# Kernel tuning notes

Hardware: AMD Instinct MI355X
Metric: run time of the kernel (lower is better)

## Reference

```python
import jax, jax.numpy as jnp
import numpy as np

# S6Layer dims: d_model=256; internal d_state=max(8,16//2)=8; expand=max(1.5,2*0.75)=1.5 -> d_inner=384
B, L, DM = 8, 4096, 256
DI, DS = 384, 8
CHUNK = 32  # seq_len > 64 path: chunked scan, state resets to 0 at every chunk (faithful to source)
EPS = 1e-5


def setup_inputs() -> dict:
    key = jax.random.key(0)
    ks = jax.random.split(key, 8)
    def w(k, shape, s=0.02):
        return jax.random.normal(k, shape, jnp.float32) * s
    return {
        "x": jax.random.normal(ks[0], (B, L, DM), jnp.float32),
        "gamma": jnp.ones((DM,), jnp.float32),
        "beta": jnp.zeros((DM,), jnp.float32),
        "W_in": w(ks[1], (3 * DI, DM)),
        "b_in": jnp.zeros((3 * DI,), jnp.float32),
        "W_dt": w(ks[2], (DI, DI)),
        "b_dt": jnp.zeros((DI,), jnp.float32),
        "A_log": jax.random.normal(ks[3], (DI, DS), jnp.float32),
        "D_vec": jax.random.normal(ks[4], (DI,), jnp.float32),
        "W_out": w(ks[5], (DM, DI)),
        "b_out": jnp.zeros((DM,), jnp.float32),
    }


def _layernorm(x, g, b):
    mu = jnp.mean(x, axis=-1, keepdims=True)
    var = jnp.mean(jnp.square(x - mu), axis=-1, keepdims=True)
    return (x - mu) * jax.lax.rsqrt(var + EPS) * g + b


def _chunked_scan(xp, dt, A):
    # xp, dt: [B, L, DI]; A: [DI, DS]. Each CHUNK-length block scans from h=0
    # (the torch code never propagates h across chunks for seq_len > 64).
    C = L // CHUNK
    xr = xp.reshape(B, C, CHUNK, DI)
    dtr = dt.reshape(B, C, CHUNK, DI)
    dA = jnp.exp(dtr[..., None] * A)              # [B, C, T, DI, DS]
    dA_t = jnp.moveaxis(dA, 2, 0)                 # [T, B, C, DI, DS]
    x_t = jnp.moveaxis(xr, 2, 0)                  # [T, B, C, DI]

    def step(h, inp):
        dA_i, x_i = inp
        h = h * dA_i + x_i[..., None]             # broadcast x over DS
        return h, jnp.sum(h, axis=-1)             # y_i: [B, C, DI]

    h0 = jnp.zeros((B, C, DI, DS), xp.dtype)
    _, ys = jax.lax.scan(step, h0, (dA_t, x_t))   # ys: [T, B, C, DI]
    return jnp.moveaxis(ys, 0, 2).reshape(B, L, DI)


def reference(x, gamma, beta, W_in, b_in, W_dt, b_dt, A_log, D_vec, W_out, b_out):
    residual = x
    xn = _layernorm(x, gamma, beta)
    xz = xn @ W_in.T + b_in                       # [B, L, 3*DI]
    x_proj, z, dt_in = jnp.split(xz, 3, axis=-1)
    x_proj = jax.nn.silu(x_proj)
    z = jax.nn.silu(z)
    dt = jax.nn.softplus(dt_in @ W_dt.T + b_dt)   # [B, L, DI]
    A = -jnp.exp(A_log)                           # [DI, DS]
    y = _chunked_scan(x_proj, dt, A)
    y = y * z + x_proj * D_vec
    return y @ W_out.T + b_out + residual
```

## Files before the change

### kernel.cpp

```cpp
#include <hip/hip_runtime.h>
#include <stdint.h>

#define B_  8
#define L_  4096
#define DM  256
#define DI  384
#define DS  8
#define M_  (B_*L_)

typedef float f32x4 __attribute__((ext_vector_type(4)));
typedef short s16x8 __attribute__((ext_vector_type(8)));

#define AS1(p) ((__attribute__((address_space(1))) void*)(p))
#define AS3(p) ((__attribute__((address_space(3))) void*)(p))

__device__ __forceinline__ unsigned short f2bf(float f) {
  union { float f; uint32_t u; } v; v.f = f;
  uint32_t r = v.u + 0x7FFFu + ((v.u >> 16) & 1u);
  return (unsigned short)(r >> 16);
}
__device__ __forceinline__ float bf2f(unsigned short h) {
  union { uint32_t u; float f; } v; v.u = ((uint32_t)h) << 16;
  return v.f;
}
__device__ __forceinline__ float silu_f(float x) {
  return x * __builtin_amdgcn_rcpf(1.f + __expf(-x));
}

__global__ __launch_bounds__(256) void cvt_kernel(
    const float* __restrict__ w0, const float* __restrict__ w2,
    const float* __restrict__ b_in,
    unsigned short* __restrict__ o0, unsigned short* __restrict__ o2,
    float* __restrict__ biasc) {
  int i = blockIdx.x * 256 + threadIdx.x;
  if (i < 3*DI*DM) o0[i] = f2bf(w0[i]);
  if (i < DM*DI)   o2[i] = f2bf(w2[i]);
  if (i < 2*DI)    biasc[i] = b_in[i];
}

__global__ __launch_bounds__(256) void prep_kernel(
    const float* __restrict__ W_in, const float* __restrict__ b_in,
    const float* __restrict__ W_dt, const float* __restrict__ b_dt,
    unsigned short* __restrict__ winb, float* __restrict__ biasc) {
  int nb = blockIdx.x;
  if (nb < DI) {
    int c = threadIdx.x;
    float acc = 0.f;
    for (int k = 0; k < DI; ++k)
      acc += W_dt[(size_t)nb*DI + k] * W_in[(size_t)(2*DI + k)*DM + c];
    winb[(size_t)(2*DI + nb)*DM + c] = f2bf(acc);
  } else {
    int n = (nb - DI)*256 + threadIdx.x;
    if (n < DI) {
      float acc = b_dt[n];
      for (int k = 0; k < DI; ++k)
        acc += W_dt[(size_t)n*DI + k] * b_in[2*DI + k];
      biasc[2*DI + n] = acc;
    }
  }
}

__global__ __launch_bounds__(256) void ln_kernel(
    const float* __restrict__ x, const float* __restrict__ gamma, const float* __restrict__ beta,
    unsigned short* __restrict__ xn) {
  int token = blockIdx.x * 4 + (threadIdx.x >> 6);
  int lane  = threadIdx.x & 63;
  const float4 v = *(const float4*)(x + (size_t)token*DM + lane*4);
  float s  = v.x + v.y + v.z + v.w;
  float ss = v.x*v.x + v.y*v.y + v.z*v.z + v.w*v.w;
  #pragma unroll
  for (int off = 32; off > 0; off >>= 1) {
    s  += __shfl_xor(s,  off, 64);
    ss += __shfl_xor(ss, off, 64);
  }
  float mean = s * (1.f/DM);
  float var  = ss * (1.f/DM) - mean*mean;
  float rstd = rsqrtf(var + 1e-5f);
  const float4 g = *(const float4*)(gamma + lane*4);
  const float4 b = *(const float4*)(beta  + lane*4);
  ushort4 o;
  o.x = f2bf((v.x - mean)*rstd*g.x + b.x);
  o.y = f2bf((v.y - mean)*rstd*g.y + b.y);
  o.z = f2bf((v.z - mean)*rstd*g.z + b.z);
  o.w = f2bf((v.w - mean)*rstd*g.w + b.w);
  *(ushort4*)(xn + (size_t)token*DM + lane*4) = o;
}

__global__ __launch_bounds__(256, 2) void s6_head(
    const unsigned short* __restrict__ xn,
    const unsigned short* __restrict__ Wb,
    const float* __restrict__ biasc,
    const float* __restrict__ A_log, const float* __restrict__ D_vec,
    unsigned short* __restrict__ yz)
{
  constexpr int K = 256, CPR = K/8;
  __shared__ unsigned short sB[64*K];
  __shared__ unsigned short sOut[3][128*64];
  const int t    = threadIdx.x;
  const int lane = t & 63;
  const int w    = t >> 6;
  const int fr   = lane & 15;
  const int fq   = lane >> 4;
  const int wm   = w * 32;

  const int q      = blockIdx.x;
  const int u      = q >> 3;
  const int mtile  = (q & 7) * 32 + (u & 31);
  const int panel  = u >> 5;
  const int mbase  = mtile * 128;
  const int chbase = panel * 64;

  const unsigned short* gA0 = xn + (size_t)(mbase + wm + fr)*K + fq*8;
  const unsigned short* gA1 = gA0 + (size_t)16*K;
  const unsigned short* sBrE = sB + (size_t)fr*K + ( fq      ^ (fr & 7))*8;
  const unsigned short* sBrO = sB + (size_t)fr*K + ((fq | 4) ^ (fr & 7))*8;

  auto STAGE = [&](int sub) {
    const int nb = sub*DI + chbase;
    #pragma unroll
    for (int i = 0; i < (64*CPR)/256; ++i) {
      int c   = i*256 + t;
      int row = c / CPR;
      int j   = c - row*CPR;
      int jp  = (j & ~7) | ((j & 7) ^ (row & 7));
      __builtin_amdgcn_global_load_lds(AS1(Wb + (size_t)(nb + row)*K + jp*8),
                                       AS3(sB + c*8), 16, 0, 0);
    }
  };
  auto KLOOP = [&](f32x4 (&acc)[2][4]) {
    #pragma unroll
    for (int mi = 0; mi < 2; ++mi)
      #pragma unroll
      for (int ni = 0; ni < 4; ++ni) acc[mi][ni] = (f32x4){0.f, 0.f, 0.f, 0.f};
    #pragma unroll
    for (int kt = 0; kt < 8; ++kt) {
      s16x8 a0 = *(const s16x8*)(gA0 + kt*32);
      s16x8 a1 = *(const s16x8*)(gA1 + kt*32);
      const unsigned short* bb = (kt & 1) ? sBrO : sBrE;
      s16x8 bfr[4];
      #pragma unroll
      for (int ni = 0; ni < 4; ++ni)
        bfr[ni] = *(const s16x8*)(bb + ni*16*K + (kt >> 1)*64);
      #pragma unroll
      for (int ni = 0; ni < 4; ++ni) {
        acc[0][ni] = __builtin_amdgcn_mfma_f32_16x16x32_bf16(a0, bfr[ni], acc[0][ni], 0, 0, 0);
        acc[1][ni] = __builtin_amdgcn_mfma_f32_16x16x32_bf16(a1, bfr[ni], acc[1][ni], 0, 0, 0);
      }
    }
  };
  auto EPI = [&](f32x4 (&acc)[2][4], int sub) {
    const int nb = sub*DI + chbase;
    const bool sl = (sub < 2);
    #pragma unroll
    for (int ni = 0; ni < 4; ++ni) {
      float bv = biasc[nb + ni*16 + fr];
      int cn = (ni*16 + fr) ^ (fq << 4);
      #pragma unroll
      for (int mi = 0; mi < 2; ++mi) {
        int rm0 = wm + mi*16 + fq*4;
        #pragma unroll
        for (int r = 0; r < 4; ++r) {
          float c = acc[mi][ni][r] + bv;
          c = sl ? silu_f(c) : ((c > 20.f) ? c : __logf(1.f + __expf(c)));
          sOut[sub][(rm0 + r)*64 + cn] = f2bf(c);
        }
      }
    }
  };

  f32x4 aP[2][4], aC[2][4];
  STAGE(0);
  __syncthreads();
  KLOOP(aP);
  __syncthreads();
  STAGE(1);
  EPI(aP, 0);
  __syncthreads();
  KLOOP(aC);
  __syncthreads();
  STAGE(2);
  EPI(aC, 1);
  __syncthreads();
  KLOOP(aP);
  EPI(aP, 2);
  __syncthreads();

  {
    const int c  = t >> 6;
    const int d  = t & 63;
    const int ch = chbase + d;
    float a[DS], h[DS];
    #pragma unroll
    for (int s = 0; s < DS; ++s) { a[s] = -__expf(A_log[ch*DS + s]); h[s] = 0.f; }
    float Dv = D_vec[ch];
    unsigned short* yzp = yz + (size_t)(mbase + c*32)*DI + ch;
    for (int tt = 0; tt < 32; ++tt) {
      int idx = (c*32 + tt)*64 + (d ^ (((tt >> 2) & 3) << 4));
      float xv  = bf2f(sOut[0][idx]);
      float zv  = bf2f(sOut[1][idx]);
      float dtv = bf2f(sOut[2][idx]);
      float y = 0.f;
      #pragma unroll
      for (int s = 0; s < DS; ++s) {
        h[s] = h[s] * __expf(dtv * a[s]) + xv;
        y += h[s];
      }
      yzp[(size_t)tt*DI] = f2bf(y * zv + xv * Dv);
    }
  }
}

__global__ __launch_bounds__(256, 3) void gemm_out(
    const unsigned short* __restrict__ A,
    const unsigned short* __restrict__ Bw,
    const float* __restrict__ bias,
    const float* __restrict__ resid, float* __restrict__ o_f)
{
  constexpr int K = 384, CPR = K/8;
  __shared__ unsigned short sB[64*K];
  float* sC = (float*)sB;

  const int t    = threadIdx.x;
  const int lane = t & 63;
  const int w    = t >> 6;
  const int fr   = lane & 15;
  const int fq   = lane >> 4;
  const int wm   = w * 32;

  const int q    = blockIdx.y * 256 + blockIdx.x;
  const int bx2  = (q & 7) * 32 + ((q >> 3) & 31);
  const int by2  = q >> 8;
  const int mbase = bx2 * 128;
  const int nbase = by2 * 64;

  #pragma unroll
  for (int i = 0; i < (64*CPR)/256; ++i) {
    int c   = i*256 + t;
    int row = c / CPR;
    int j   = c - row*CPR;
    int jp  = (j & ~7) | ((j & 7) ^ (row & 7));
    __builtin_amdgcn_global_load_lds(AS1(Bw + (size_t)(nbase + row)*K + jp*8),
                                     AS3(sB + c*8), 16, 0, 0);
  }

  const unsigned short* sBrE = sB + (size_t)fr*K + ( fq      ^ (fr & 7))*8;
  const unsigned short* sBrO = sB + (size_t)fr*K + ((fq | 4) ^ (fr & 7))*8;

  float bvv[4];
  #pragma unroll
  for (int ni = 0; ni < 4; ++ni) bvv[ni] = bias[nbase + ni*16 + fr];

  __syncthreads();

  const unsigned short* gA0 = A + (size_t)(mbase + wm + fr)*K + fq*8;
  const unsigned short* gA1 = gA0 + (size_t)16*K;

  f32x4 acc[2][4];
  #pragma unroll
  for (int mi = 0; mi < 2; ++mi)
    #pragma unroll
    for (int ni = 0; ni < 4; ++ni) acc[mi][ni] = (f32x4){0.f, 0.f, 0.f, 0.f};

  #pragma unroll
  for (int kt = 0; kt < 12; ++kt) {
    s16x8 a0 = *(const s16x8*)(gA0 + kt*32);
    s16x8 a1 = *(const s16x8*)(gA1 + kt*32);
    const unsigned short* bb = (kt & 1) ? sBrO : sBrE;
    s16x8 bfr[4];
    #pragma unroll
    for (int ni = 0; ni < 4; ++ni)
      bfr[ni] = *(const s16x8*)(bb + ni*16*K + (kt >> 1)*64);
    #pragma unroll
    for (int ni = 0; ni < 4; ++ni) {
      acc[0][ni] = __builtin_amdgcn_mfma_f32_16x16x32_bf16(a0, bfr[ni], acc[0][ni], 0, 0, 0);
      acc[1][ni] = __builtin_amdgcn_mfma_f32_16x16x32_bf16(a1, bfr[ni], acc[1][ni], 0, 0, 0);
    }
  }

  __syncthreads();

  #pragma unroll
  for (int ni = 0; ni < 4; ++ni)
    #pragma unroll
    for (int mi = 0; mi < 2; ++mi)
      #pragma unroll
      for (int r = 0; r < 4; ++r)
        sC[(wm + mi*16 + fq*4 + r)*72 + ni*16 + fr] = acc[mi][ni][r] + bvv[ni];

  __syncthreads();

  const int rr = t >> 4, cl = (t & 15) * 4;
  #pragma unroll
  for (int it = 0; it < 8; ++it) {
    int row = rr + it*16;
    const float4 c  = *(const float4*)&sC[row*72 + cl];
    const float4 rv = *(const float4*)(resid + (size_t)(mbase + row)*DM + nbase + cl);
    float4 o;
    o.x = c.x + rv.x; o.y = c.y + rv.y; o.z = c.z + rv.z; o.w = c.w + rv.w;
    *(float4*)(o_f + (size_t)(mbase + row)*DM + nbase + cl) = o;
  }
}

extern "C" void kernel_launch(void* const* d_in, const int* in_sizes, int n_in,
                              void* d_out, int out_size, void* d_ws, size_t ws_size,
                              hipStream_t stream) {
  const float* x     = (const float*)d_in[0];
  const float* gamma = (const float*)d_in[1];
  const float* beta  = (const float*)d_in[2];
  const float* W_in  = (const float*)d_in[3];
  const float* b_in  = (const float*)d_in[4];
  const float* W_dt  = (const float*)d_in[5];
  const float* b_dt  = (const float*)d_in[6];
  const float* A_log = (const float*)d_in[7];
  const float* D_vec = (const float*)d_in[8];
  const float* W_out = (const float*)d_in[9];
  const float* b_out = (const float*)d_in[10];
  float* out = (float*)d_out;

  char* ws = (char*)d_ws;
  size_t off = 0;
  auto alloc = [&](size_t bytes) -> char* {
    char* p = ws + off; off += (bytes + 255) & ~(size_t)255; return p;
  };
  unsigned short* xn    = (unsigned short*)alloc((size_t)M_*DM*2);
  unsigned short* yzb   = (unsigned short*)alloc((size_t)M_*DI*2);
  unsigned short* winb  = (unsigned short*)alloc((size_t)3*DI*DM*2);
  unsigned short* woutb = (unsigned short*)alloc((size_t)DM*DI*2);
  float*          biasc = (float*)alloc((size_t)3*DI*4);

  cvt_kernel<<<dim3((3*DI*DM + 255)/256), 256, 0, stream>>>(W_in, W_out, b_in, winb, woutb, biasc);
  prep_kernel<<<dim3(DI + 2), 256, 0, stream>>>(W_in, b_in, W_dt, b_dt, winb, biasc);
  ln_kernel<<<dim3(M_/4), 256, 0, stream>>>(x, gamma, beta, xn);
  s6_head<<<dim3(6 * 256), 256, 0, stream>>>(xn, winb, biasc, A_log, D_vec, yzb);
  gemm_out<<<dim3(256, DM/64), 256, 0, stream>>>(yzb, woutb, b_out, x, out);
}
```

Baseline: 209.8 us.

## Split-K weight fusion prep, preload A fragments, use exp2 in scan

The serial prep kernel that folds W_dt into W_in (384-step dot per thread) is split into a 4-way split-K kernel plus a reduction kernel, so the preprocessing runs on more blocks with shorter dependency chains. In s6_head, the A-operand fragments are loaded once into registers and reused across the three GEMM sub-passes instead of being reloaded from global memory each time. The scan uses exp2f with A prescaled by log2(e). These changes add an extra launch, scratch memory, and more register pressure in s6_head.

```diff
diff --git a/kernel.cpp b/kernel.cpp
--- a/kernel.cpp
+++ b/kernel.cpp
@@ -38,26 +38,43 @@
   if (i < 2*DI)    biasc[i] = b_in[i];
 }
 
-__global__ __launch_bounds__(256) void prep_kernel(
+__global__ __launch_bounds__(256) void prep1_kernel(
     const float* __restrict__ W_in, const float* __restrict__ b_in,
-    const float* __restrict__ W_dt, const float* __restrict__ b_dt,
+    const float* __restrict__ W_dt,
+    float* __restrict__ scr, float* __restrict__ bscr) {
+  const int n  = blockIdx.x;
+  const int kc = blockIdx.y;
+  const int c  = threadIdx.x;
+  const int kb = kc * 96;
+  const float* wd = W_dt + (size_t)n*DI + kb;
+  const float* wi = W_in + (size_t)(2*DI + kb)*DM + c;
+  float p0 = 0.f, p1 = 0.f, p2 = 0.f, p3 = 0.f;
+  #pragma unroll
+  for (int k = 0; k < 96; k += 4) {
+    p0 += wd[k+0] * wi[(size_t)(k+0)*DM];
+    p1 += wd[k+1] * wi[(size_t)(k+1)*DM];
+    p2 += wd[k+2] * wi[(size_t)(k+2)*DM];
+    p3 += wd[k+3] * wi[(size_t)(k+3)*DM];
+  }
+  scr[(size_t)(n*4 + kc)*256 + c] = (p0 + p1) + (p2 + p3);
+  if (c < 64) {
+    float p = wd[c] * b_in[2*DI + kb + c];
+    if (c < 32) p += wd[64 + c] * b_in[2*DI + kb + 64 + c];
+    #pragma unroll
+    for (int off = 32; off > 0; off >>= 1) p += __shfl_down(p, off, 64);
+    if (c == 0) bscr[n*4 + kc] = p;
+  }
+}
+
+__global__ __launch_bounds__(256) void prep2_kernel(
+    const float* __restrict__ scr, const float* __restrict__ bscr,
+    const float* __restrict__ b_dt,
     unsigned short* __restrict__ winb, float* __restrict__ biasc) {
-  int nb = blockIdx.x;
-  if (nb < DI) {
-    int c = threadIdx.x;
-    float acc = 0.f;
-    for (int k = 0; k < DI; ++k)
-      acc += W_dt[(size_t)nb*DI + k] * W_in[(size_t)(2*DI + k)*DM + c];
-    winb[(size_t)(2*DI + nb)*DM + c] = f2bf(acc);
-  } else {
-    int n = (nb - DI)*256 + threadIdx.x;
-    if (n < DI) {
-      float acc = b_dt[n];
-      for (int k = 0; k < DI; ++k)
-        acc += W_dt[(size_t)n*DI + k] * b_in[2*DI + k];
-      biasc[2*DI + n] = acc;
-    }
-  }
+  const int n = blockIdx.x, c = threadIdx.x;
+  const float* s = scr + (size_t)n*4*256 + c;
+  winb[(size_t)(2*DI + n)*DM + c] = f2bf((s[0] + s[256]) + (s[512] + s[768]));
+  if (c == 0)
+    biasc[2*DI + n] = b_dt[n] + ((bscr[n*4] + bscr[n*4+1]) + (bscr[n*4+2] + bscr[n*4+3]));
 }
 
 __global__ __launch_bounds__(256) void ln_kernel(
@@ -115,6 +132,13 @@
   const unsigned short* sBrE = sB + (size_t)fr*K + ( fq      ^ (fr & 7))*8;
   const unsigned short* sBrO = sB + (size_t)fr*K + ((fq | 4) ^ (fr & 7))*8;
 
+  s16x8 afr[8][2];
+  #pragma unroll
+  for (int kt = 0; kt < 8; ++kt) {
+    afr[kt][0] = *(const s16x8*)(gA0 + kt*32);
+    afr[kt][1] = *(const s16x8*)(gA1 + kt*32);
+  }
+
   auto STAGE = [&](int sub) {
     const int nb = sub*DI + chbase;
     #pragma unroll
@@ -134,8 +158,6 @@
       for (int ni = 0; ni < 4; ++ni) acc[mi][ni] = (f32x4){0.f, 0.f, 0.f, 0.f};
     #pragma unroll
     for (int kt = 0; kt < 8; ++kt) {
-      s16x8 a0 = *(const s16x8*)(gA0 + kt*32);
-      s16x8 a1 = *(const s16x8*)(gA1 + kt*32);
       const unsigned short* bb = (kt & 1) ? sBrO : sBrE;
       s16x8 bfr[4];
       #pragma unroll
@@ -143,8 +165,8 @@
         bfr[ni] = *(const s16x8*)(bb + ni*16*K + (kt >> 1)*64);
       #pragma unroll
       for (int ni = 0; ni < 4; ++ni) {
-        acc[0][ni] = __builtin_amdgcn_mfma_f32_16x16x32_bf16(a0, bfr[ni], acc[0][ni], 0, 0, 0);
-        acc[1][ni] = __builtin_amdgcn_mfma_f32_16x16x32_bf16(a1, bfr[ni], acc[1][ni], 0, 0, 0);
+        acc[0][ni] = __builtin_amdgcn_mfma_f32_16x16x32_bf16(afr[kt][0], bfr[ni], acc[0][ni], 0, 0, 0);
+        acc[1][ni] = __builtin_amdgcn_mfma_f32_16x16x32_bf16(afr[kt][1], bfr[ni], acc[1][ni], 0, 0, 0);
       }
     }
   };
@@ -189,9 +211,12 @@
     const int c  = t >> 6;
     const int d  = t & 63;
     const int ch = chbase + d;
-    float a[DS], h[DS];
-    #pragma unroll
-    for (int s = 0; s < DS; ++s) { a[s] = -__expf(A_log[ch*DS + s]); h[s] = 0.f; }
+    float a2[DS], h[DS];
+    #pragma unroll
+    for (int s = 0; s < DS; ++s) {
+      a2[s] = -__expf(A_log[ch*DS + s]) * 1.44269504f;
+      h[s] = 0.f;
+    }
     float Dv = D_vec[ch];
     unsigned short* yzp = yz + (size_t)(mbase + c*32)*DI + ch;
     for (int tt = 0; tt < 32; ++tt) {
@@ -202,7 +227,7 @@
       float y = 0.f;
       #pragma unroll
       for (int s = 0; s < DS; ++s) {
-        h[s] = h[s] * __expf(dtv * a[s]) + xv;
+        h[s] = h[s] * exp2f(dtv * a2[s]) + xv;
         y += h[s];
       }
       yzp[(size_t)tt*DI] = f2bf(y * zv + xv * Dv);
@@ -327,9 +352,12 @@
   unsigned short* winb  = (unsigned short*)alloc((size_t)3*DI*DM*2);
   unsigned short* woutb = (unsigned short*)alloc((size_t)DM*DI*2);
   float*          biasc = (float*)alloc((size_t)3*DI*4);
+  float*          scr   = (float*)alloc((size_t)DI*4*256*4);
+  float*          bscr  = (float*)alloc((size_t)DI*4*4);
 
   cvt_kernel<<<dim3((3*DI*DM + 255)/256), 256, 0, stream>>>(W_in, W_out, b_in, winb, woutb, biasc);
-  prep_kernel<<<dim3(DI + 2), 256, 0, stream>>>(W_in, b_in, W_dt, b_dt, winb, biasc);
+  prep1_kernel<<<dim3(DI, 4), 256, 0, stream>>>(W_in, b_in, W_dt, scr, bscr);
+  prep2_kernel<<<dim3(DI), 256, 0, stream>>>(scr, bscr, b_dt, winb, biasc);
   ln_kernel<<<dim3(M_/4), 256, 0, stream>>>(x, gamma, beta, xn);
   s6_head<<<dim3(6 * 256), 256, 0, stream>>>(xn, winb, biasc, A_log, D_vec, yzb);
   gemm_out<<<dim3(256, DM/64), 256, 0, stream>>>(yzb, woutb, b_out, x, out);
```

After: 198.5 us. 5.4% less time.
